# Kernel optimization log

Hardware: AMD Instinct MI355X
Metric: run time of the kernel (lower is better)

The kernel has to match this reference:

```python
import jax, jax.numpy as jnp
import numpy as np

N = 20000      # num_nodes
E = 320000     # num_edges (avg degree 16)
HID = 256      # hid_dim
H = 4          # attention heads
D = HID // H   # per-head dim (concat heads -> HID)
L = 2          # nGAT_layer
OUT = 12       # out_dim / pred_len (decoder steps)
NEG_SLOPE = 0.2


def setup_inputs() -> dict:
    key = jax.random.key(0)
    ks = jax.random.split(key, 16)
    s = 0.05
    nrm = lambda k, shape: jax.random.normal(k, shape, jnp.float32) * s
    return dict(
        x=nrm(ks[0], (N, HID)),
        edge_index=jax.random.randint(ks[1], (2, E), 0, N, dtype=jnp.int32),
        # GATv2Conv params per layer (stacked over L layers)
        gat_w_src=nrm(ks[2], (L, HID, H * D)),
        gat_w_dst=nrm(ks[3], (L, HID, H * D)),
        gat_att=nrm(ks[4], (L, H, D)),
        gat_bias=nrm(ks[5], (L, H * D)),
        # decoder_mlp: Linear(1 + HID -> HID)
        mlp_w=nrm(ks[6], (HID, 1 + HID)),
        mlp_b=nrm(ks[7], (HID,)),
        # nn.LSTM (1 layer, input HID, hidden HID), torch gate order i,f,g,o
        lstm_w_ih=nrm(ks[8], (4 * HID, HID)),
        lstm_w_hh=nrm(ks[9], (4 * HID, HID)),
        lstm_b_ih=nrm(ks[10], (4 * HID,)),
        lstm_b_hh=nrm(ks[11], (4 * HID,)),
        # decoder_init_proj: Linear(HID -> 1); decoder_output_proj: Linear(HID -> 1)
        init_w=nrm(ks[12], (1, HID)),
        init_b=nrm(ks[13], (1,)),
        out_w=nrm(ks[14], (1, HID)),
        out_b=nrm(ks[15], (1,)),
    )


def _gatv2_layer(x, src, dst, w_src, w_dst, att, bias):
    n = x.shape[0]
    xl = (x @ w_src).reshape(n, H, D)   # source-side projection
    xr = (x @ w_dst).reshape(n, H, D)   # destination-side projection
    # GATv2: e_ij = a^T LeakyReLU(Wl x_j + Wr x_i)
    e = jax.nn.leaky_relu(xl[src] + xr[dst], NEG_SLOPE)        # [E,H,D]
    logits = jnp.einsum('ehd,hd->eh', e, att)                   # [E,H]
    # edge softmax over incoming edges of each destination node
    m = jax.ops.segment_max(logits, dst, num_segments=n)        # [N,H]
    ex = jnp.exp(logits - m[dst])
    denom = jax.ops.segment_sum(ex, dst, num_segments=n)
    alpha = ex / denom[dst]                                     # [E,H]
    out = jax.ops.segment_sum(xl[src] * alpha[:, :, None], dst, num_segments=n)
    return out.reshape(n, H * D) + bias


def reference(x, edge_index, gat_w_src, gat_w_dst, gat_att, gat_bias,
              mlp_w, mlp_b, lstm_w_ih, lstm_w_hh, lstm_b_ih, lstm_b_hh,
              init_w, init_b, out_w, out_b):
    src, dst = edge_index[0], edge_index[1]
    # stacked GAT blocks: GATv2Conv + ELU (element == 2)
    for l in range(L):
        x = _gatv2_layer(x, src, dst, gat_w_src[l], gat_w_dst[l], gat_att[l], gat_bias[l])
        x = jax.nn.elu(x)
    # recurrent LSTM decoder, batch = nodes, seq step by step
    ctx = x                      # encoder_context
    h = x                        # h_0 = x (num_layers = 1)
    c = jnp.zeros_like(x)        # c_0 = 0
    prev = x @ init_w.T + init_b  # [N,1]
    outs = []
    for _ in range(OUT):
        dec_in = jnp.concatenate([prev, ctx], axis=1) @ mlp_w.T + mlp_b  # [N,HID]
        gates = dec_in @ lstm_w_ih.T + lstm_b_ih + h @ lstm_w_hh.T + lstm_b_hh
        i_g, f_g, g_g, o_g = jnp.split(gates, 4, axis=1)
        i_g = jax.nn.sigmoid(i_g)
        f_g = jax.nn.sigmoid(f_g)
        o_g = jax.nn.sigmoid(o_g)
        g_g = jnp.tanh(g_g)
        c = f_g * c + i_g * g_g
        h = o_g * jnp.tanh(c)
        prev = h @ out_w.T + out_b  # [N,1]
        outs.append(prev)
    return jnp.concatenate(outs, axis=1)  # [N, OUT]
```

## Files before the change

kernel.cpp:

```cpp
#include <hip/hip_runtime.h>
#include <hip/hip_bf16.h>

#define NN 20000
#define NE 320000
#define TOUT 12
#define DEGMAX 96
#define MR 48
#define NBLK 417

typedef __bf16 bf16x8 __attribute__((ext_vector_type(8)));
typedef float float4v __attribute__((ext_vector_type(4)));

#define LD8(p) (*(const bf16x8*)(p))
#define MFMA16(a,b,c) __builtin_amdgcn_mfma_f32_16x16x32_bf16((a),(b),(c),0,0,0)

__device__ __forceinline__ float bf2f(const __hip_bfloat16 v){ return __bfloat162float(v); }
__device__ __forceinline__ __hip_bfloat16 f2bf(float v){ return __float2bfloat16(v); }
__device__ __forceinline__ float sigmoidr_(float x){ return __builtin_amdgcn_rcpf(1.f + __expf(-x)); }
__device__ __forceinline__ float tanhr_(float x){ return 1.f - 2.f*__builtin_amdgcn_rcpf(__expf(2.f*x) + 1.f); }
__device__ __forceinline__ float rdf(const void* p, int i, int f32){
  return f32 ? ((const float*)p)[i] : __bfloat162float(((const __hip_bfloat16*)p)[i]);
}

__global__ void k_detect(const void* xraw, int* flag){
  __shared__ int cnt;
  if(threadIdx.x == 0) cnt = 0;
  __syncthreads();
  const unsigned* w = (const unsigned*)xraw;
  int local = 0;
  for(int i = threadIdx.x; i < 4096; i += 256){
    unsigned b = (w[i] >> 8) & 0x7F;
    if(b >= 0x33 && b <= 0x3F) local++;
  }
  atomicAdd(&cnt, local);
  __syncthreads();
  if(threadIdx.x == 0) *flag = (cnt > 2048) ? 0 : 1;
}

__global__ void k_fail(float* out, int n){
  int i = blockIdx.x*256 + threadIdx.x;
  if(i < n) out[i] = 256.0f;
}

__global__ void k_count(const int* __restrict__ dst, int* __restrict__ deg){
  int e = blockIdx.x*256 + threadIdx.x;
  if(e < NE){
    unsigned d = (unsigned)dst[e];
    if(d < NN) atomicAdd(&deg[d], 1);
  }
}

__global__ void k_scan(const int* __restrict__ deg, int* __restrict__ offp, int* __restrict__ cursor){
  __shared__ int part[256];
  __shared__ int excl[257];
  const int CH = (NN + 255)/256;
  int tid = threadIdx.x;
  int lo = tid*CH;
  int hi = lo + CH; if(hi > NN) hi = NN;
  int s = 0;
  for(int i=lo;i<hi;i++) s += deg[i];
  part[tid] = s;
  __syncthreads();
  if(tid == 0){
    int run = 0;
    for(int i=0;i<256;i++){ excl[i] = run; run += part[i]; }
    excl[256] = run;
  }
  __syncthreads();
  int run = excl[tid];
  for(int i=lo;i<hi;i++){ offp[i] = run; cursor[i] = run; run += deg[i]; }
  if(tid == 0) offp[NN] = excl[256];
}

__global__ void k_fill(const int* __restrict__ src, const int* __restrict__ dst,
                       int* __restrict__ cursor, int* __restrict__ csr_src){
  int e = blockIdx.x*256 + threadIdx.x;
  if(e >= NE) return;
  unsigned d = (unsigned)dst[e];
  if(d >= NN) return;
  unsigned p = (unsigned)atomicAdd(&cursor[d], 1);
  if(p < NE){
    unsigned sv = (unsigned)src[e];
    csr_src[p] = (sv < NN) ? (int)sv : 0;
  }
}

__global__ void k_prep(const void* __restrict__ w_src, const void* __restrict__ w_dst,
                       const void* __restrict__ w_hh, const void* __restrict__ wih,
                       const void* __restrict__ mlp_w, const int* __restrict__ flag,
                       __hip_bfloat16* __restrict__ wsrcT, __hip_bfloat16* __restrict__ wdstT,
                       __hip_bfloat16* __restrict__ whhp, __hip_bfloat16* __restrict__ wihb,
                       __hip_bfloat16* __restrict__ mlpT){
  int tid = blockIdx.x*256 + threadIdx.x;
  int f = *flag;
  if(tid < 131072){
    int l = tid >> 16, r = tid & 65535, o = r >> 8, i = r & 255;
    wsrcT[tid] = f2bf(rdf(w_src, l*65536 + i*256 + o, f));
    wdstT[tid] = f2bf(rdf(w_dst, l*65536 + i*256 + o, f));
  }
  if(tid < 262144){
    whhp[tid] = f2bf(rdf(w_hh, tid, f));
    wihb[tid] = f2bf(rdf(wih, tid, f));
  }
  if(tid < 65536){
    int k = tid >> 8, j = tid & 255;
    mlpT[tid] = f2bf(rdf(mlp_w, j*257 + 1 + k, f));
  }
}

__global__ void k_prep_ub(const void* __restrict__ wih, const void* __restrict__ mlp_w,
                          const void* __restrict__ mlp_b,
                          const void* __restrict__ b_ih, const void* __restrict__ b_hh,
                          const void* __restrict__ att, const void* __restrict__ gbias,
                          const void* __restrict__ init_w, const void* __restrict__ init_b,
                          const void* __restrict__ out_w, const void* __restrict__ out_b,
                          const int* __restrict__ flag,
                          float* __restrict__ u, float* __restrict__ bc,
                          float* __restrict__ attf, float* __restrict__ gbiasf,
                          float* __restrict__ initwf, float* __restrict__ outwf,
                          float* __restrict__ sc){
  __shared__ float su[256], sb[256];
  int g = blockIdx.x, j = threadIdx.x, f = *flag;
  float w = rdf(wih, g*256 + j, f);
  su[j] = w * rdf(mlp_w, j*257, f);
  sb[j] = w * rdf(mlp_b, j, f);
  if(g < 2){
    int i = g*256 + j;
    attf[i] = rdf(att, i, f);
    gbiasf[i] = rdf(gbias, i, f);
  }
  if(g == 0){
    initwf[j] = rdf(init_w, j, f);
    outwf[j]  = rdf(out_w, j, f);
    if(j == 0){ sc[0] = rdf(init_b, 0, f); sc[1] = rdf(out_b, 0, f); }
  }
  __syncthreads();
  for(int s=128; s>0; s>>=1){
    if(j < s){ su[j] += su[j+s]; sb[j] += sb[j+s]; }
    __syncthreads();
  }
  if(j == 0){ u[g] = su[0]; bc[g] = sb[0] + rdf(b_ih, g, f) + rdf(b_hh, g, f); }
}

__global__ void k_pack(const __hip_bfloat16* __restrict__ Wpl, const __hip_bfloat16* __restrict__ Wcpl,
                       __hip_bfloat16* __restrict__ WhhP, __hip_bfloat16* __restrict__ WcP){
  int idx = blockIdx.x*256 + threadIdx.x;
  if(idx >= 32768) return;
  int cs = idx >> 12;
  int kslot = (idx >> 9) & 7;
  int nt = (idx >> 6) & 7;
  int lane = idx & 63;
  int l16 = lane & 15, quad = lane >> 4;
  int brow = (nt>>1)*256 + cs*32 + (nt&1)*16 + l16;
  int srcofs = brow*256 + kslot*32 + quad*8;
  int dst = idx*8;
  *(bf16x8*)(WhhP + dst) = LD8(Wpl + srcofs);
  *(bf16x8*)(WcP + dst)  = LD8(Wcpl + srcofs);
}

__global__ void k_pack2(const __hip_bfloat16* __restrict__ wsrcT,
                        const __hip_bfloat16* __restrict__ wdstT,
                        __hip_bfloat16* __restrict__ wprojP){
  int idx = blockIdx.x*256 + threadIdx.x;
  if(idx >= 32768) return;
  int m = idx >> 13;
  int fi = idx & 8191;
  int l = m >> 1, role = m & 1;
  int kidx = fi >> 10;
  int nt = (fi >> 6) & 15;
  int lane = fi & 63;
  int l16 = lane & 15, quad = lane >> 4;
  const __hip_bfloat16* src = (role ? wdstT : wsrcT) + l*65536;
  int srcofs = (nt*16 + l16)*256 + kidx*32 + quad*8;
  *(bf16x8*)(wprojP + (size_t)m*65536 + fi*8) = LD8(src + srcofs);
}

__global__ __launch_bounds__(256) void k_gemm_nt_bf(const __hip_bfloat16* __restrict__ A,
                                                    const __hip_bfloat16* __restrict__ B,
                                                    __hip_bfloat16* __restrict__ Cb, int M){
  int wave = threadIdx.x >> 6;
  int lane = threadIdx.x & 63;
  int l16 = lane & 15, quad = lane >> 4, quad8 = quad*8;
  int mBase = blockIdx.x*64 + wave*16;
  int nBase = blockIdx.y*64;
  int arow = mBase + l16; if(arow >= M) arow = M-1;
  const __hip_bfloat16* aptr = A + (size_t)arow*256 + quad8;
  float4v acc[4];
  #pragma unroll
  for(int nt=0;nt<4;nt++){ acc[nt][0]=0.f; acc[nt][1]=0.f; acc[nt][2]=0.f; acc[nt][3]=0.f; }
  for(int k0=0;k0<256;k0+=32){
    bf16x8 a = LD8(aptr + k0);
    #pragma unroll
    for(int nt=0;nt<4;nt++){
      const __hip_bfloat16* bptr = B + (size_t)(nBase + nt*16 + l16)*256 + k0 + quad8;
      acc[nt] = MFMA16(a, LD8(bptr), acc[nt]);
    }
  }
  #pragma unroll
  for(int nt=0;nt<4;nt++){
    int col = nBase + nt*16 + l16;
    #pragma unroll
    for(int r=0;r<4;r++){
      int row = mBase + quad*4 + r;
      if(row < M) Cb[(size_t)row*256 + col] = f2bf(acc[nt][r]);
    }
  }
}

__global__ __launch_bounds__(512, 2) void k_gemm_dual(__hip_bfloat16* __restrict__ P,
                                                      const void* __restrict__ xraw,
                                                      const int* __restrict__ flag,
                                                      int layer0,
                                                      const __hip_bfloat16* __restrict__ BsrcP,
                                                      const __hip_bfloat16* __restrict__ BdstP,
                                                      __hip_bfloat16* __restrict__ Q){
  __shared__ __hip_bfloat16 sA[64*264];
  int tid = threadIdx.x;
  int mBase = blockIdx.x*64;
  {
    int r = tid >> 3;
    int c0 = (tid & 7)*32;
    int grow = mBase + r; if(grow >= NN) grow = NN-1;
    if(layer0){
      int f = *flag;
      #pragma unroll
      for(int j=0;j<32;j++) sA[r*264 + c0 + j] = f2bf(rdf(xraw, grow*256 + c0 + j, f));
    }else{
      const __hip_bfloat16* srcp = P + (size_t)grow*256 + c0;
      #pragma unroll
      for(int j=0;j<4;j++) *(bf16x8*)(&sA[r*264 + c0 + j*8]) = LD8(srcp + j*8);
    }
  }
  __syncthreads();
  int w8 = tid >> 6;
  int w = w8 & 3;
  int role = w8 >> 2;
  int lane = tid&63, l16 = lane&15, quad = lane>>4, quad8 = quad*8;
  const __hip_bfloat16* B = role ? BdstP : BsrcP;
  __hip_bfloat16* C = role ? P : Q;
  const __hip_bfloat16* arow = &sA[(w*16 + l16)*264 + quad8];
  float4v acc[16];
  #pragma unroll
  for(int nt=0;nt<16;nt++){ acc[nt][0]=0.f; acc[nt][1]=0.f; acc[nt][2]=0.f; acc[nt][3]=0.f; }
  for(int kidx=0;kidx<8;kidx++){
    bf16x8 a = *(const bf16x8*)(arow + kidx*32);
    const __hip_bfloat16* bbase = B + (kidx<<13) + (lane<<3);
    #pragma unroll
    for(int nt=0;nt<16;nt++)
      acc[nt] = MFMA16(a, LD8(bbase + (nt<<9)), acc[nt]);
  }
  #pragma unroll
  for(int nt=0;nt<16;nt++){
    int col = nt*16 + l16;
    #pragma unroll
    for(int r=0;r<4;r++){
      int row = mBase + w*16 + quad*4 + r;
      if(row < NN) C[(size_t)row*256 + col] = f2bf(acc[nt][r]);
    }
  }
}

__global__ __launch_bounds__(256) void k_node_fused(const __hip_bfloat16* __restrict__ Q,
                                                    __hip_bfloat16* __restrict__ P,
                                                    const int* __restrict__ offp,
                                                    const int* __restrict__ csr_src,
                                                    const float* __restrict__ attf,
                                                    const float* __restrict__ gbiasf){
  __shared__ float slog[DEGMAX*4];
  __shared__ int ssrc[DEGMAX];
  int node = blockIdx.x;
  int tid = threadIdx.x;
  int s0 = offp[node], s1 = offp[node+1];
  if(s0 < 0) s0 = 0; if(s0 > NE) s0 = NE;
  if(s1 < s0) s1 = s0; if(s1 > NE) s1 = NE;
  int deg = s1 - s0; if(deg > DEGMAX) deg = DEGMAX;
  if(tid < deg){
    unsigned sv = (unsigned)csr_src[s0 + tid];
    ssrc[tid] = (sv < NN) ? (int)sv : 0;
  }
  __syncthreads();
  int w = tid>>6, lane = tid&63;
  int eSlot = lane>>4, li = lane&15;
  float prl[16], attl[16];
  #pragma unroll
  for(int h=0;h<4;h++)
    #pragma unroll
    for(int j=0;j<4;j++){
      int d = h*64 + j*16 + li;
      prl[h*4+j]  = bf2f(P[(size_t)node*256 + d]);
      attl[h*4+j] = attf[d];
    }
  for(int base=0; base<deg; base+=16){
    int e = base + w*4 + eSlot;
    bool valid = (e < deg);
    const __hip_bfloat16* pl = Q + (size_t)ssrc[valid ? e : 0]*256;
    float part[4];
    #pragma unroll
    for(int h=0;h<4;h++){
      float p = 0.f;
      #pragma unroll
      for(int j=0;j<4;j++){
        int d = h*64 + j*16 + li;
        float v = bf2f(pl[d]) + prl[h*4+j];
        v = (v > 0.f) ? v : 0.2f*v;
        p += v * attl[h*4+j];
      }
      part[h] = p;
    }
    #pragma unroll
    for(int h=0;h<4;h++){
      part[h] += __shfl_xor(part[h], 1, 64);
      part[h] += __shfl_xor(part[h], 2, 64);
      part[h] += __shfl_xor(part[h], 4, 64);
      part[h] += __shfl_xor(part[h], 8, 64);
    }
    if(li == 0 && valid){
      #pragma unroll
      for(int h=0;h<4;h++) slog[e*4+h] = part[h];
    }
  }
  __syncthreads();
  if(tid < 4){
    int hh = tid;
    float m = -1e30f;
    for(int i=0;i<deg;i++) m = fmaxf(m, slog[i*4+hh]);
    float den = 0.f;
    for(int i=0;i<deg;i++) den += __expf(slog[i*4+hh] - m);
    float inv = (den > 0.f) ? 1.f/den : 0.f;
    for(int i=0;i<deg;i++) slog[i*4+hh] = __expf(slog[i*4+hh] - m)*inv;
  }
  __syncthreads();
  int d = tid, hd = d>>6;
  float acc = 0.f;
  for(int i=0;i<deg;i++) acc += slog[i*4+hd] * bf2f(Q[(size_t)ssrc[i]*256 + d]);
  acc += gbiasf[d];
  acc = (acc > 0.f) ? acc : (__expf(acc) - 1.f);
  P[(size_t)node*256 + d] = f2bf(acc);
}

__global__ __launch_bounds__(512, 2) void k_lstm12(const __hip_bfloat16* __restrict__ ctx,
                                                   const __hip_bfloat16* __restrict__ WcP,
                                                   const __hip_bfloat16* __restrict__ WhhP,
                                                   const float* __restrict__ u_vec,
                                                   const float* __restrict__ bc_vec,
                                                   const float* __restrict__ initwf,
                                                   const float* __restrict__ outwf,
                                                   const float* __restrict__ sc,
                                                   float* __restrict__ out){
  __shared__ __hip_bfloat16 sgxW[8*12*512];
  __shared__ __hip_bfloat16 sh[MR*264];
  __shared__ float spart[512];
  __shared__ float spartw[MR*8];
  __shared__ float sprev[MR];
  int tid = threadIdx.x;
  int mBase = blockIdx.x*MR;
  int cs = tid>>6, lane = tid&63, l16 = lane&15, quad = lane>>4, quad8 = quad*8;
  int phase = (blockIdx.x >> 3) & 7;
  int wavebase = cs*6144 + lane*8;
  #pragma unroll
  for(int p=0;p<2;p++){
    int r = p*32 + (tid >> 4);
    if(r < MR){
      int grow = mBase + r; if(grow >= NN) grow = NN-1;
      int c0 = (tid & 15)*16;
      const __hip_bfloat16* srcp = ctx + (size_t)grow*256 + c0;
      *(bf16x8*)(&sh[r*264 + c0])     = LD8(srcp);
      *(bf16x8*)(&sh[r*264 + c0 + 8]) = LD8(srcp + 8);
    }
  }
  __syncthreads();
  #pragma unroll
  for(int p=0;p<2;p++){
    int r = p*32 + (tid >> 4);
    int c0 = (tid & 15)*16;
    float part = 0.f;
    if(r < MR){
      #pragma unroll
      for(int j=0;j<16;j++) part += bf2f(sh[r*264 + c0 + j]) * initwf[c0 + j];
    }
    spart[tid] = part;
    __syncthreads();
    if(tid < 32 && p*32 + tid < MR){
      float s = 0.f;
      #pragma unroll
      for(int j=0;j<16;j++) s += spart[tid*16 + j];
      sprev[p*32 + tid] = s + sc[0];
    }
    __syncthreads();
  }
  float ureg[8], owreg[2];
  #pragma unroll
  for(int g=0;g<4;g++)
    #pragma unroll
    for(int tc=0;tc<2;tc++) ureg[g*2+tc] = u_vec[g*256 + cs*32 + tc*16 + l16];
  #pragma unroll
  for(int tc=0;tc<2;tc++) owreg[tc] = outwf[cs*32 + tc*16 + l16];
  float outb = sc[1];
  {
    float4v acc[24];
    #pragma unroll
    for(int nt=0;nt<24;nt++){ acc[nt][0]=0.f; acc[nt][1]=0.f; acc[nt][2]=0.f; acc[nt][3]=0.f; }
    #pragma unroll 2
    for(int ki=0;ki<8;ki++){
      int kidx = (ki + phase) & 7;
      int k0 = kidx*32;
      bf16x8 a0 = *(const bf16x8*)(&sh[l16*264 + k0 + quad8]);
      bf16x8 a1 = *(const bf16x8*)(&sh[(16 + l16)*264 + k0 + quad8]);
      bf16x8 a2 = *(const bf16x8*)(&sh[(32 + l16)*264 + k0 + quad8]);
      const __hip_bfloat16* bbase = WcP + (((cs<<3) + kidx)<<12) + (lane<<3);
      #pragma unroll
      for(int nt=0;nt<8;nt++){
        bf16x8 b = LD8(bbase + (nt<<9));
        acc[nt]    = MFMA16(a0, b, acc[nt]);
        acc[8+nt]  = MFMA16(a1, b, acc[8+nt]);
        acc[16+nt] = MFMA16(a2, b, acc[16+nt]);
      }
    }
    #pragma unroll
    for(int rt=0;rt<3;rt++)
      #pragma unroll
      for(int tc=0;tc<2;tc++)
        #pragma unroll
        for(int half=0;half<2;half++){
          bf16x8 v;
          #pragma unroll
          for(int rr=0;rr<2;rr++)
            #pragma unroll
            for(int g=0;g<4;g++){
              int r = half*2 + rr;
              float bcv = bc_vec[g*256 + cs*32 + tc*16 + l16];
              v[rr*4+g] = (__bf16)f2bf(acc[rt*8 + g*2 + tc][r] + bcv);
            }
          int cp = (rt*2+tc)*2 + half;
          *(bf16x8*)(&sgxW[wavebase + cp*512]) = v;
        }
  }
  __syncthreads();
  float creg[24];
  #pragma unroll
  for(int i=0;i<24;i++) creg[i] = 0.f;
  for(int step=0; step<TOUT; step++){
    float4v acc[24];
    #pragma unroll
    for(int nt=0;nt<24;nt++){ acc[nt][0]=0.f; acc[nt][1]=0.f; acc[nt][2]=0.f; acc[nt][3]=0.f; }
    #pragma unroll 2
    for(int ki=0;ki<8;ki++){
      int kidx = (ki + phase) & 7;
      int k0 = kidx*32;
      bf16x8 a0 = *(const bf16x8*)(&sh[l16*264 + k0 + quad8]);
      bf16x8 a1 = *(const bf16x8*)(&sh[(16 + l16)*264 + k0 + quad8]);
      bf16x8 a2 = *(const bf16x8*)(&sh[(32 + l16)*264 + k0 + quad8]);
      const __hip_bfloat16* bbase = WhhP + (((cs<<3) + kidx)<<12) + (lane<<3);
      #pragma unroll
      for(int nt=0;nt<8;nt++){
        bf16x8 b = LD8(bbase + (nt<<9));
        acc[nt]    = MFMA16(a0, b, acc[nt]);
        acc[8+nt]  = MFMA16(a1, b, acc[8+nt]);
        acc[16+nt] = MFMA16(a2, b, acc[16+nt]);
      }
    }
    __syncthreads();
    float hsum[12];
    #pragma unroll
    for(int i=0;i<12;i++) hsum[i] = 0.f;
    #pragma unroll
    for(int rt=0;rt<3;rt++)
      #pragma unroll
      for(int tc=0;tc<2;tc++){
        int col = cs*32 + tc*16 + l16;
        int cpb = (rt*2+tc)*2;
        bf16x8 ga = *(const bf16x8*)(&sgxW[wavebase + cpb*512]);
        bf16x8 gb = *(const bf16x8*)(&sgxW[wavebase + (cpb+1)*512]);
        #pragma unroll
        for(int r=0;r<4;r++){
          int row = rt*16 + quad*4 + r;
          float p = sprev[row];
          int jb = (r&1)*4;
          float gx0, gx1, gx2, gx3;
          if(r < 2){
            gx0 = bf2f((__hip_bfloat16)ga[jb]);   gx1 = bf2f((__hip_bfloat16)ga[jb+1]);
            gx2 = bf2f((__hip_bfloat16)ga[jb+2]); gx3 = bf2f((__hip_bfloat16)ga[jb+3]);
          }else{
            gx0 = bf2f((__hip_bfloat16)gb[jb]);   gx1 = bf2f((__hip_bfloat16)gb[jb+1]);
            gx2 = bf2f((__hip_bfloat16)gb[jb+2]); gx3 = bf2f((__hip_bfloat16)gb[jb+3]);
          }
          float g0 = acc[rt*8 + tc][r]     + gx0 + p*ureg[tc];
          float g1 = acc[rt*8 + 2 + tc][r] + gx1 + p*ureg[2+tc];
          float g2 = acc[rt*8 + 4 + tc][r] + gx2 + p*ureg[4+tc];
          float g3 = acc[rt*8 + 6 + tc][r] + gx3 + p*ureg[6+tc];
          float iv = sigmoidr_(g0), fv = sigmoidr_(g1);
          float gv = tanhr_(g2),    ov = sigmoidr_(g3);
          float cn = fv*creg[rt*8 + tc*4 + r] + iv*gv;
          creg[rt*8 + tc*4 + r] = cn;
          float hn = ov * tanhr_(cn);
          sh[row*264 + col] = f2bf(hn);
          hsum[rt*4 + r] += hn * owreg[tc];
        }
      }
    #pragma unroll
    for(int rr=0;rr<12;rr++){
      hsum[rr] += __shfl_xor(hsum[rr], 1, 64);
      hsum[rr] += __shfl_xor(hsum[rr], 2, 64);
      hsum[rr] += __shfl_xor(hsum[rr], 4, 64);
      hsum[rr] += __shfl_xor(hsum[rr], 8, 64);
    }
    if(l16 == 0){
      #pragma unroll
      for(int rt=0;rt<3;rt++)
        #pragma unroll
        for(int r=0;r<4;r++)
          spartw[(rt*16 + quad*4 + r)*8 + cs] = hsum[rt*4 + r];
    }
    __syncthreads();
    if(tid < MR){
      float s = outb;
      #pragma unroll
      for(int c=0;c<8;c++) s += spartw[tid*8 + c];
      sprev[tid] = s;
      int row = mBase + tid;
      if(row < NN) out[(size_t)row*TOUT + step] = s;
    }
  }
}

extern "C" void kernel_launch(void* const* d_in, const int* in_sizes, int n_in,
                              void* d_out, int out_size, void* d_ws, size_t ws_size,
                              hipStream_t stream){
  const void* x      = d_in[0];
  const int*  ei     = (const int*)d_in[1];
  const void* w_src  = d_in[2];
  const void* w_dst  = d_in[3];
  const void* att    = d_in[4];
  const void* gbias  = d_in[5];
  const void* mlp_w  = d_in[6];
  const void* mlp_b  = d_in[7];
  const void* w_ih   = d_in[8];
  const void* w_hh   = d_in[9];
  const void* b_ih   = d_in[10];
  const void* b_hh   = d_in[11];
  const void* init_w = d_in[12];
  const void* init_b = d_in[13];
  const void* out_w  = d_in[14];
  const void* out_b  = d_in[15];
  float* out = (float*)d_out;
  const int* srcp = ei;
  const int* dstp = ei + NE;
  (void)in_sizes; (void)n_in;

  char* ws = (char*)d_ws;
  size_t off = 0;
  auto alloc = [&](size_t bytes)->void*{
    void* p = ws + off;
    off += (bytes + 255) & ~(size_t)255;
    return p;
  };
  __hip_bfloat16* P = (__hip_bfloat16*)alloc((size_t)NN*256*2);
  __hip_bfloat16* Q = (__hip_bfloat16*)alloc((size_t)NN*256*2);
  int* deg      = (int*)alloc((size_t)NN*4);
  int* offp     = (int*)alloc((size_t)(NN+1)*4);
  int* cursor   = (int*)alloc((size_t)NN*4);
  int* csr_src  = (int*)alloc((size_t)NE*4);
  __hip_bfloat16* wsrcT   = (__hip_bfloat16*)alloc((size_t)131072*2);
  __hip_bfloat16* wdstT   = (__hip_bfloat16*)alloc((size_t)131072*2);
  __hip_bfloat16* wprojP  = (__hip_bfloat16*)alloc((size_t)4*65536*2);
  __hip_bfloat16* whh_pl  = (__hip_bfloat16*)alloc((size_t)262144*2);
  __hip_bfloat16* Wc_pl   = (__hip_bfloat16*)alloc((size_t)262144*2);
  __hip_bfloat16* WhhP    = (__hip_bfloat16*)alloc((size_t)262144*2);
  __hip_bfloat16* WcP     = (__hip_bfloat16*)alloc((size_t)262144*2);
  __hip_bfloat16* wihb    = (__hip_bfloat16*)alloc((size_t)262144*2);
  __hip_bfloat16* mlpT    = (__hip_bfloat16*)alloc((size_t)65536*2);
  float* u_vec  = (float*)alloc(1024*4);
  float* bc_vec = (float*)alloc(1024*4);
  float* attf   = (float*)alloc(512*4);
  float* gbiasf = (float*)alloc(512*4);
  float* initwf = (float*)alloc(256*4);
  float* outwf  = (float*)alloc(256*4);
  float* sc     = (float*)alloc(2*4);
  int*   flag   = (int*)alloc(4);

  if(off > ws_size){
    k_fail<<<(out_size + 255)/256, 256, 0, stream>>>(out, out_size);
    return;
  }

  k_detect<<<1, 256, 0, stream>>>(x, flag);
  hipMemsetAsync(deg, 0, (size_t)NN*4, stream);
  hipMemsetAsync(csr_src, 0xFF, (size_t)NE*4, stream);
  k_count<<<NE/256, 256, 0, stream>>>(dstp, deg);
  k_scan<<<1, 256, 0, stream>>>(deg, offp, cursor);
  k_fill<<<NE/256, 256, 0, stream>>>(srcp, dstp, cursor, csr_src);
  k_prep<<<1024, 256, 0, stream>>>(w_src, w_dst, w_hh, w_ih, mlp_w, flag,
                                   wsrcT, wdstT, whh_pl, wihb, mlpT);
  {
    dim3 gwc(16, 4);
    k_gemm_nt_bf<<<gwc, 256, 0, stream>>>(wihb, mlpT, Wc_pl, 1024);
  }
  k_pack<<<128, 256, 0, stream>>>(whh_pl, Wc_pl, WhhP, WcP);
  k_pack2<<<128, 256, 0, stream>>>(wsrcT, wdstT, wprojP);
  k_prep_ub<<<1024, 256, 0, stream>>>(w_ih, mlp_w, mlp_b, b_ih, b_hh, att, gbias,
                                      init_w, init_b, out_w, out_b, flag,
                                      u_vec, bc_vec, attf, gbiasf, initwf, outwf, sc);

  for(int l=0;l<2;l++){
    k_gemm_dual<<<313, 512, 0, stream>>>(P, x, flag, (l == 0) ? 1 : 0,
                                         wprojP + (size_t)(l*2)*65536,
                                         wprojP + (size_t)(l*2+1)*65536, Q);
    k_node_fused<<<NN, 256, 0, stream>>>(Q, P, offp, csr_src, attf + l*256, gbiasf + l*256);
  }

  k_lstm12<<<NBLK, 512, 0, stream>>>(P, WcP, WhhP, u_vec, bc_vec, initwf, outwf, sc, out);
}
```

Measured before the change: 666.9 us.

## Shrink LSTM tile to 32 rows for higher occupancy and parallelize edge softmax

The LSTM decoder kernel now processes 32 rows per block instead of 48, using 625 blocks with launch bounds allowing 4 blocks per CU. It cuts accumulator registers, keeps one gate-input chunk in registers and reuses the gate buffer as scratch to shrink LDS. Separately, the per-node edge softmax now uses all 256 threads (one wavefront per head) with shuffle reductions instead of 4 serial threads. The smaller tile means each weight load feeds fewer MFMAs, so weight traffic per row goes up.

```diff
diff --git a/kernel.cpp b/kernel.cpp
--- a/kernel.cpp
+++ b/kernel.cpp
@@ -5,8 +5,8 @@
 #define NE 320000
 #define TOUT 12
 #define DEGMAX 96
-#define MR 48
-#define NBLK 417
+#define MR 32
+#define NBLK 625
 
 typedef __bf16 bf16x8 __attribute__((ext_vector_type(8)));
 typedef float float4v __attribute__((ext_vector_type(4)));
@@ -320,14 +320,19 @@
     }
   }
   __syncthreads();
-  if(tid < 4){
-    int hh = tid;
+  {
+    int hh = tid >> 6;
+    int li64 = tid & 63;
     float m = -1e30f;
-    for(int i=0;i<deg;i++) m = fmaxf(m, slog[i*4+hh]);
+    for(int i=li64; i<deg; i+=64) m = fmaxf(m, slog[i*4+hh]);
+    #pragma unroll
+    for(int s=1; s<64; s<<=1) m = fmaxf(m, __shfl_xor(m, s, 64));
     float den = 0.f;
-    for(int i=0;i<deg;i++) den += __expf(slog[i*4+hh] - m);
+    for(int i=li64; i<deg; i+=64) den += __expf(slog[i*4+hh] - m);
+    #pragma unroll
+    for(int s=1; s<64; s<<=1) den += __shfl_xor(den, s, 64);
     float inv = (den > 0.f) ? 1.f/den : 0.f;
-    for(int i=0;i<deg;i++) slog[i*4+hh] = __expf(slog[i*4+hh] - m)*inv;
+    for(int i=li64; i<deg; i+=64) slog[i*4+hh] = __expf(slog[i*4+hh] - m)*inv;
   }
   __syncthreads();
   int d = tid, hd = d>>6;
@@ -338,7 +343,7 @@
   P[(size_t)node*256 + d] = f2bf(acc);
 }
 
-__global__ __launch_bounds__(512, 2) void k_lstm12(const __hip_bfloat16* __restrict__ ctx,
+__global__ __launch_bounds__(512, 4) void k_lstm32(const __hip_bfloat16* __restrict__ ctx,
                                                    const __hip_bfloat16* __restrict__ WcP,
                                                    const __hip_bfloat16* __restrict__ WhhP,
                                                    const float* __restrict__ u_vec,
@@ -347,44 +352,37 @@
                                                    const float* __restrict__ outwf,
                                                    const float* __restrict__ sc,
                                                    float* __restrict__ out){
-  __shared__ __hip_bfloat16 sgxW[8*12*512];
+  __shared__ __hip_bfloat16 sgxW[7*512*8];
   __shared__ __hip_bfloat16 sh[MR*264];
-  __shared__ float spart[512];
   __shared__ float spartw[MR*8];
   __shared__ float sprev[MR];
+  float* spart = (float*)sgxW;
   int tid = threadIdx.x;
   int mBase = blockIdx.x*MR;
   int cs = tid>>6, lane = tid&63, l16 = lane&15, quad = lane>>4, quad8 = quad*8;
   int phase = (blockIdx.x >> 3) & 7;
-  int wavebase = cs*6144 + lane*8;
-  #pragma unroll
-  for(int p=0;p<2;p++){
-    int r = p*32 + (tid >> 4);
-    if(r < MR){
-      int grow = mBase + r; if(grow >= NN) grow = NN-1;
-      int c0 = (tid & 15)*16;
-      const __hip_bfloat16* srcp = ctx + (size_t)grow*256 + c0;
-      *(bf16x8*)(&sh[r*264 + c0])     = LD8(srcp);
-      *(bf16x8*)(&sh[r*264 + c0 + 8]) = LD8(srcp + 8);
-    }
-  }
-  __syncthreads();
-  #pragma unroll
-  for(int p=0;p<2;p++){
-    int r = p*32 + (tid >> 4);
+  {
+    int r = tid >> 4;
+    int grow = mBase + r; if(grow >= NN) grow = NN-1;
+    int c0 = (tid & 15)*16;
+    const __hip_bfloat16* srcp = ctx + (size_t)grow*256 + c0;
+    *(bf16x8*)(&sh[r*264 + c0])     = LD8(srcp);
+    *(bf16x8*)(&sh[r*264 + c0 + 8]) = LD8(srcp + 8);
+  }
+  __syncthreads();
+  {
+    int r = tid >> 4;
     int c0 = (tid & 15)*16;
     float part = 0.f;
-    if(r < MR){
-      #pragma unroll
-      for(int j=0;j<16;j++) part += bf2f(sh[r*264 + c0 + j]) * initwf[c0 + j];
-    }
+    #pragma unroll
+    for(int j=0;j<16;j++) part += bf2f(sh[r*264 + c0 + j]) * initwf[c0 + j];
     spart[tid] = part;
     __syncthreads();
-    if(tid < 32 && p*32 + tid < MR){
+    if(tid < MR){
       float s = 0.f;
       #pragma unroll
       for(int j=0;j<16;j++) s += spart[tid*16 + j];
-      sprev[p*32 + tid] = s + sc[0];
+      sprev[tid] = s + sc[0];
     }
     __syncthreads();
   }
@@ -396,28 +394,27 @@
   #pragma unroll
   for(int tc=0;tc<2;tc++) owreg[tc] = outwf[cs*32 + tc*16 + l16];
   float outb = sc[1];
+  bf16x8 gx7;
   {
-    float4v acc[24];
-    #pragma unroll
-    for(int nt=0;nt<24;nt++){ acc[nt][0]=0.f; acc[nt][1]=0.f; acc[nt][2]=0.f; acc[nt][3]=0.f; }
+    float4v acc[16];
+    #pragma unroll
+    for(int nt=0;nt<16;nt++){ acc[nt][0]=0.f; acc[nt][1]=0.f; acc[nt][2]=0.f; acc[nt][3]=0.f; }
     #pragma unroll 2
     for(int ki=0;ki<8;ki++){
       int kidx = (ki + phase) & 7;
       int k0 = kidx*32;
       bf16x8 a0 = *(const bf16x8*)(&sh[l16*264 + k0 + quad8]);
       bf16x8 a1 = *(const bf16x8*)(&sh[(16 + l16)*264 + k0 + quad8]);
-      bf16x8 a2 = *(const bf16x8*)(&sh[(32 + l16)*264 + k0 + quad8]);
       const __hip_bfloat16* bbase = WcP + (((cs<<3) + kidx)<<12) + (lane<<3);
       #pragma unroll
       for(int nt=0;nt<8;nt++){
         bf16x8 b = LD8(bbase + (nt<<9));
-        acc[nt]    = MFMA16(a0, b, acc[nt]);
-        acc[8+nt]  = MFMA16(a1, b, acc[8+nt]);
-        acc[16+nt] = MFMA16(a2, b, acc[16+nt]);
+        acc[nt]   = MFMA16(a0, b, acc[nt]);
+        acc[8+nt] = MFMA16(a1, b, acc[8+nt]);
       }
     }
     #pragma unroll
-    for(int rt=0;rt<3;rt++)
+    for(int rt=0;rt<2;rt++)
       #pragma unroll
       for(int tc=0;tc<2;tc++)
         #pragma unroll
@@ -432,45 +429,46 @@
               v[rr*4+g] = (__bf16)f2bf(acc[rt*8 + g*2 + tc][r] + bcv);
             }
           int cp = (rt*2+tc)*2 + half;
-          *(bf16x8*)(&sgxW[wavebase + cp*512]) = v;
+          if(cp == 7) gx7 = v;
+          else *(bf16x8*)(&sgxW[cp*4096 + tid*8]) = v;
         }
   }
   __syncthreads();
-  float creg[24];
-  #pragma unroll
-  for(int i=0;i<24;i++) creg[i] = 0.f;
+  float creg[16];
+  #pragma unroll
+  for(int i=0;i<16;i++) creg[i] = 0.f;
   for(int step=0; step<TOUT; step++){
-    float4v acc[24];
-    #pragma unroll
-    for(int nt=0;nt<24;nt++){ acc[nt][0]=0.f; acc[nt][1]=0.f; acc[nt][2]=0.f; acc[nt][3]=0.f; }
+    float4v acc[16];
+    #pragma unroll
+    for(int nt=0;nt<16;nt++){ acc[nt][0]=0.f; acc[nt][1]=0.f; acc[nt][2]=0.f; acc[nt][3]=0.f; }
     #pragma unroll 2
     for(int ki=0;ki<8;ki++){
       int kidx = (ki + phase) & 7;
       int k0 = kidx*32;
       bf16x8 a0 = *(const bf16x8*)(&sh[l16*264 + k0 + quad8]);
       bf16x8 a1 = *(const bf16x8*)(&sh[(16 + l16)*264 + k0 + quad8]);
-      bf16x8 a2 = *(const bf16x8*)(&sh[(32 + l16)*264 + k0 + quad8]);
       const __hip_bfloat16* bbase = WhhP + (((cs<<3) + kidx)<<12) + (lane<<3);
       #pragma unroll
       for(int nt=0;nt<8;nt++){
         bf16x8 b = LD8(bbase + (nt<<9));
-        acc[nt]    = MFMA16(a0, b, acc[nt]);
-        acc[8+nt]  = MFMA16(a1, b, acc[8+nt]);
-        acc[16+nt] = MFMA16(a2, b, acc[16+nt]);
+        acc[nt]   = MFMA16(a0, b, acc[nt]);
+        acc[8+nt] = MFMA16(a1, b, acc[8+nt]);
       }
     }
     __syncthreads();
-    float hsum[12];
-    #pragma unroll
-    for(int i=0;i<12;i++) hsum[i] = 0.f;
-    #pragma unroll
-    for(int rt=0;rt<3;rt++)
+    float hsum[8];
+    #pragma unroll
+    for(int i=0;i<8;i++) hsum[i] = 0.f;
+    #pragma unroll
+    for(int rt=0;rt<2;rt++)
       #pragma unroll
       for(int tc=0;tc<2;tc++){
         int col = cs*32 + tc*16 + l16;
         int cpb = (rt*2+tc)*2;
-        bf16x8 ga = *(const bf16x8*)(&sgxW[wavebase + cpb*512]);
-        bf16x8 gb = *(const bf16x8*)(&sgxW[wavebase + (cpb+1)*512]);
+        bf16x8 ga = *(const bf16x8*)(&sgxW[cpb*4096 + tid*8]);
+        bf16x8 gb;
+        if(cpb + 1 == 7) gb = gx7;
+        else gb = *(const bf16x8*)(&sgxW[(cpb+1)*4096 + tid*8]);
         #pragma unroll
         for(int r=0;r<4;r++){
           int row = rt*16 + quad*4 + r;
@@ -498,7 +496,7 @@
         }
       }
     #pragma unroll
-    for(int rr=0;rr<12;rr++){
+    for(int rr=0;rr<8;rr++){
       hsum[rr] += __shfl_xor(hsum[rr], 1, 64);
       hsum[rr] += __shfl_xor(hsum[rr], 2, 64);
       hsum[rr] += __shfl_xor(hsum[rr], 4, 64);
@@ -506,7 +504,7 @@
     }
     if(l16 == 0){
       #pragma unroll
-      for(int rt=0;rt<3;rt++)
+      for(int rt=0;rt<2;rt++)
         #pragma unroll
         for(int r=0;r<4;r++)
           spartw[(rt*16 + quad*4 + r)*8 + cs] = hsum[rt*4 + r];
@@ -608,5 +606,5 @@
     k_node_fused<<<NN, 256, 0, stream>>>(Q, P, offp, csr_src, attf + l*256, gbiasf + l*256);
   }
 
-  k_lstm12<<<NBLK, 512, 0, stream>>>(P, WcP, WhhP, u_vec, bc_vec, initwf, outwf, sc, out);
-}
+  k_lstm32<<<NBLK, 512, 0, stream>>>(P, WcP, WhhP, u_vec, bc_vec, initwf, outwf, sc, out);
+}
```

After: 705.6 us. 5.8% more time.

## Enlarge LSTM row tile to 80 with global spill of precomputed gates; parallelize softmax

Applied to the files above, without the earlier changes.

The LSTM decoder kernel now processes 80 rows per block instead of 48, which cuts the grid to 250 blocks and amortizes each block's weight-matrix loads over more rows. Because the precomputed input-gate values no longer fit in LDS, part of them goes to a global scratch buffer and is reloaded every step. The GAT node kernel's edge softmax now runs across all 256 threads with wave shuffles instead of only 4 serial threads. The trade-offs are much higher register pressure (40 accumulator tiles plus 40 cell-state registers) and extra global traffic per step.

```diff
diff --git a/kernel.cpp b/kernel.cpp
--- a/kernel.cpp
+++ b/kernel.cpp
@@ -5,8 +5,10 @@
 #define NE 320000
 #define TOUT 12
 #define DEGMAX 96
-#define MR 48
-#define NBLK 417
+#define MR 80
+#define NBLK 250
+#define NCHL 14
+#define NCHG 6
 
 typedef __bf16 bf16x8 __attribute__((ext_vector_type(8)));
 typedef float float4v __attribute__((ext_vector_type(4)));
@@ -320,14 +322,19 @@
     }
   }
   __syncthreads();
-  if(tid < 4){
-    int hh = tid;
+  {
+    int hh = tid >> 6;
+    int li64 = tid & 63;
     float m = -1e30f;
-    for(int i=0;i<deg;i++) m = fmaxf(m, slog[i*4+hh]);
+    for(int i=li64; i<deg; i+=64) m = fmaxf(m, slog[i*4+hh]);
+    #pragma unroll
+    for(int s=1; s<64; s<<=1) m = fmaxf(m, __shfl_xor(m, s, 64));
     float den = 0.f;
-    for(int i=0;i<deg;i++) den += __expf(slog[i*4+hh] - m);
+    for(int i=li64; i<deg; i+=64) den += __expf(slog[i*4+hh] - m);
+    #pragma unroll
+    for(int s=1; s<64; s<<=1) den += __shfl_xor(den, s, 64);
     float inv = (den > 0.f) ? 1.f/den : 0.f;
-    for(int i=0;i<deg;i++) slog[i*4+hh] = __expf(slog[i*4+hh] - m)*inv;
+    for(int i=li64; i<deg; i+=64) slog[i*4+hh] = __expf(slog[i*4+hh] - m)*inv;
   }
   __syncthreads();
   int d = tid, hd = d>>6;
@@ -338,7 +345,7 @@
   P[(size_t)node*256 + d] = f2bf(acc);
 }
 
-__global__ __launch_bounds__(512, 2) void k_lstm12(const __hip_bfloat16* __restrict__ ctx,
+__global__ __launch_bounds__(512, 2) void k_lstm80(const __hip_bfloat16* __restrict__ ctx,
                                                    const __hip_bfloat16* __restrict__ WcP,
                                                    const __hip_bfloat16* __restrict__ WhhP,
                                                    const float* __restrict__ u_vec,
@@ -346,31 +353,31 @@
                                                    const float* __restrict__ initwf,
                                                    const float* __restrict__ outwf,
                                                    const float* __restrict__ sc,
+                                                   __hip_bfloat16* __restrict__ gxg,
                                                    float* __restrict__ out){
-  __shared__ __hip_bfloat16 sgxW[8*12*512];
+  __shared__ __hip_bfloat16 sgx[NCHL*4096];
   __shared__ __hip_bfloat16 sh[MR*264];
-  __shared__ float spart[512];
   __shared__ float spartw[MR*8];
   __shared__ float sprev[MR];
+  float* spart = (float*)sgx;
   int tid = threadIdx.x;
   int mBase = blockIdx.x*MR;
   int cs = tid>>6, lane = tid&63, l16 = lane&15, quad = lane>>4, quad8 = quad*8;
   int phase = (blockIdx.x >> 3) & 7;
-  int wavebase = cs*6144 + lane*8;
-  #pragma unroll
-  for(int p=0;p<2;p++){
+  __hip_bfloat16* gxb = gxg + (size_t)blockIdx.x*(NCHG*4096);
+  #pragma unroll
+  for(int p=0;p<3;p++){
     int r = p*32 + (tid >> 4);
     if(r < MR){
-      int grow = mBase + r; if(grow >= NN) grow = NN-1;
       int c0 = (tid & 15)*16;
-      const __hip_bfloat16* srcp = ctx + (size_t)grow*256 + c0;
+      const __hip_bfloat16* srcp = ctx + (size_t)(mBase + r)*256 + c0;
       *(bf16x8*)(&sh[r*264 + c0])     = LD8(srcp);
       *(bf16x8*)(&sh[r*264 + c0 + 8]) = LD8(srcp + 8);
     }
   }
   __syncthreads();
   #pragma unroll
-  for(int p=0;p<2;p++){
+  for(int p=0;p<3;p++){
     int r = p*32 + (tid >> 4);
     int c0 = (tid & 15)*16;
     float part = 0.f;
@@ -397,9 +404,14 @@
   for(int tc=0;tc<2;tc++) owreg[tc] = outwf[cs*32 + tc*16 + l16];
   float outb = sc[1];
   {
-    float4v acc[24];
-    #pragma unroll
-    for(int nt=0;nt<24;nt++){ acc[nt][0]=0.f; acc[nt][1]=0.f; acc[nt][2]=0.f; acc[nt][3]=0.f; }
+    float bcl[8];
+    #pragma unroll
+    for(int g=0;g<4;g++)
+      #pragma unroll
+      for(int tc=0;tc<2;tc++) bcl[g*2+tc] = bc_vec[g*256 + cs*32 + tc*16 + l16];
+    float4v acc[40];
+    #pragma unroll
+    for(int nt=0;nt<40;nt++){ acc[nt][0]=0.f; acc[nt][1]=0.f; acc[nt][2]=0.f; acc[nt][3]=0.f; }
     #pragma unroll 2
     for(int ki=0;ki<8;ki++){
       int kidx = (ki + phase) & 7;
@@ -407,6 +419,8 @@
       bf16x8 a0 = *(const bf16x8*)(&sh[l16*264 + k0 + quad8]);
       bf16x8 a1 = *(const bf16x8*)(&sh[(16 + l16)*264 + k0 + quad8]);
       bf16x8 a2 = *(const bf16x8*)(&sh[(32 + l16)*264 + k0 + quad8]);
+      bf16x8 a3 = *(const bf16x8*)(&sh[(48 + l16)*264 + k0 + quad8]);
+      bf16x8 a4 = *(const bf16x8*)(&sh[(64 + l16)*264 + k0 + quad8]);
       const __hip_bfloat16* bbase = WcP + (((cs<<3) + kidx)<<12) + (lane<<3);
       #pragma unroll
       for(int nt=0;nt<8;nt++){
@@ -414,10 +428,12 @@
         acc[nt]    = MFMA16(a0, b, acc[nt]);
         acc[8+nt]  = MFMA16(a1, b, acc[8+nt]);
         acc[16+nt] = MFMA16(a2, b, acc[16+nt]);
+        acc[24+nt] = MFMA16(a3, b, acc[24+nt]);
+        acc[32+nt] = MFMA16(a4, b, acc[32+nt]);
       }
     }
     #pragma unroll
-    for(int rt=0;rt<3;rt++)
+    for(int rt=0;rt<5;rt++)
       #pragma unroll
       for(int tc=0;tc<2;tc++)
         #pragma unroll
@@ -428,21 +444,21 @@
             #pragma unroll
             for(int g=0;g<4;g++){
               int r = half*2 + rr;
-              float bcv = bc_vec[g*256 + cs*32 + tc*16 + l16];
-              v[rr*4+g] = (__bf16)f2bf(acc[rt*8 + g*2 + tc][r] + bcv);
+              v[rr*4+g] = (__bf16)f2bf(acc[rt*8 + g*2 + tc][r] + bcl[g*2+tc]);
             }
           int cp = (rt*2+tc)*2 + half;
-          *(bf16x8*)(&sgxW[wavebase + cp*512]) = v;
+          if(cp < NCHL) *(bf16x8*)(&sgx[cp*4096 + tid*8]) = v;
+          else          *(bf16x8*)(gxb + (cp-NCHL)*4096 + tid*8) = v;
         }
   }
   __syncthreads();
-  float creg[24];
-  #pragma unroll
-  for(int i=0;i<24;i++) creg[i] = 0.f;
+  float creg[40];
+  #pragma unroll
+  for(int i=0;i<40;i++) creg[i] = 0.f;
   for(int step=0; step<TOUT; step++){
-    float4v acc[24];
-    #pragma unroll
-    for(int nt=0;nt<24;nt++){ acc[nt][0]=0.f; acc[nt][1]=0.f; acc[nt][2]=0.f; acc[nt][3]=0.f; }
+    float4v acc[40];
+    #pragma unroll
+    for(int nt=0;nt<40;nt++){ acc[nt][0]=0.f; acc[nt][1]=0.f; acc[nt][2]=0.f; acc[nt][3]=0.f; }
     #pragma unroll 2
     for(int ki=0;ki<8;ki++){
       int kidx = (ki + phase) & 7;
@@ -450,6 +466,8 @@
       bf16x8 a0 = *(const bf16x8*)(&sh[l16*264 + k0 + quad8]);
       bf16x8 a1 = *(const bf16x8*)(&sh[(16 + l16)*264 + k0 + quad8]);
       bf16x8 a2 = *(const bf16x8*)(&sh[(32 + l16)*264 + k0 + quad8]);
+      bf16x8 a3 = *(const bf16x8*)(&sh[(48 + l16)*264 + k0 + quad8]);
+      bf16x8 a4 = *(const bf16x8*)(&sh[(64 + l16)*264 + k0 + quad8]);
       const __hip_bfloat16* bbase = WhhP + (((cs<<3) + kidx)<<12) + (lane<<3);
       #pragma unroll
       for(int nt=0;nt<8;nt++){
@@ -457,20 +475,24 @@
         acc[nt]    = MFMA16(a0, b, acc[nt]);
         acc[8+nt]  = MFMA16(a1, b, acc[8+nt]);
         acc[16+nt] = MFMA16(a2, b, acc[16+nt]);
+        acc[24+nt] = MFMA16(a3, b, acc[24+nt]);
+        acc[32+nt] = MFMA16(a4, b, acc[32+nt]);
       }
     }
+    bf16x8 gg[NCHG];
+    #pragma unroll
+    for(int j=0;j<NCHG;j++) gg[j] = LD8(gxb + j*4096 + tid*8);
     __syncthreads();
-    float hsum[12];
-    #pragma unroll
-    for(int i=0;i<12;i++) hsum[i] = 0.f;
-    #pragma unroll
-    for(int rt=0;rt<3;rt++)
+    #pragma unroll
+    for(int rt=0;rt<5;rt++){
+      float hsum[4];
+      hsum[0]=0.f; hsum[1]=0.f; hsum[2]=0.f; hsum[3]=0.f;
       #pragma unroll
       for(int tc=0;tc<2;tc++){
         int col = cs*32 + tc*16 + l16;
         int cpb = (rt*2+tc)*2;
-        bf16x8 ga = *(const bf16x8*)(&sgxW[wavebase + cpb*512]);
-        bf16x8 gb = *(const bf16x8*)(&sgxW[wavebase + (cpb+1)*512]);
+        bf16x8 ga = (cpb   < NCHL) ? *(const bf16x8*)(&sgx[cpb*4096 + tid*8])     : gg[cpb-NCHL];
+        bf16x8 gb = (cpb+1 < NCHL) ? *(const bf16x8*)(&sgx[(cpb+1)*4096 + tid*8]) : gg[cpb+1-NCHL];
         #pragma unroll
         for(int r=0;r<4;r++){
           int row = rt*16 + quad*4 + r;
@@ -494,22 +516,21 @@
           creg[rt*8 + tc*4 + r] = cn;
           float hn = ov * tanhr_(cn);
           sh[row*264 + col] = f2bf(hn);
-          hsum[rt*4 + r] += hn * owreg[tc];
+          hsum[r] += hn * owreg[tc];
         }
       }
-    #pragma unroll
-    for(int rr=0;rr<12;rr++){
-      hsum[rr] += __shfl_xor(hsum[rr], 1, 64);
-      hsum[rr] += __shfl_xor(hsum[rr], 2, 64);
-      hsum[rr] += __shfl_xor(hsum[rr], 4, 64);
-      hsum[rr] += __shfl_xor(hsum[rr], 8, 64);
-    }
-    if(l16 == 0){
-      #pragma unroll
-      for(int rt=0;rt<3;rt++)
+      #pragma unroll
+      for(int r=0;r<4;r++){
+        hsum[r] += __shfl_xor(hsum[r], 1, 64);
+        hsum[r] += __shfl_xor(hsum[r], 2, 64);
+        hsum[r] += __shfl_xor(hsum[r], 4, 64);
+        hsum[r] += __shfl_xor(hsum[r], 8, 64);
+      }
+      if(l16 == 0){
         #pragma unroll
         for(int r=0;r<4;r++)
-          spartw[(rt*16 + quad*4 + r)*8 + cs] = hsum[rt*4 + r];
+          spartw[(rt*16 + quad*4 + r)*8 + cs] = hsum[r];
+      }
     }
     __syncthreads();
     if(tid < MR){
@@ -517,8 +538,7 @@
       #pragma unroll
       for(int c=0;c<8;c++) s += spartw[tid*8 + c];
       sprev[tid] = s;
-      int row = mBase + tid;
-      if(row < NN) out[(size_t)row*TOUT + step] = s;
+      out[(size_t)(mBase + tid)*TOUT + step] = s;
     }
   }
 }
@@ -569,6 +589,7 @@
   __hip_bfloat16* WcP     = (__hip_bfloat16*)alloc((size_t)262144*2);
   __hip_bfloat16* wihb    = (__hip_bfloat16*)alloc((size_t)262144*2);
   __hip_bfloat16* mlpT    = (__hip_bfloat16*)alloc((size_t)65536*2);
+  __hip_bfloat16* gxg     = (__hip_bfloat16*)alloc((size_t)NBLK*NCHG*4096*2);
   float* u_vec  = (float*)alloc(1024*4);
   float* bc_vec = (float*)alloc(1024*4);
   float* attf   = (float*)alloc(512*4);
@@ -608,5 +629,5 @@
     k_node_fused<<<NN, 256, 0, stream>>>(Q, P, offp, csr_src, attf + l*256, gbiasf + l*256);
   }
 
-  k_lstm12<<<NBLK, 512, 0, stream>>>(P, WcP, WhhP, u_vec, bc_vec, initwf, outwf, sc, out);
-}
+  k_lstm80<<<NBLK, 512, 0, stream>>>(P, WcP, WhhP, u_vec, bc_vec, initwf, outwf, sc, gxg, out);
+}
```

New measurement: 721.0 us. 8.1% more time.
